# Optimization experiments

Measured on AMD Instinct MI355X. Metric: run time of the kernel, lower is better.

Reference implementation:

```python
import jax, jax.numpy as jnp
import numpy as np

MARGIN = 0.5

def setup_inputs() -> dict:
    key = jax.random.key(0)
    k1, k2 = jax.random.split(key)
    inputs = jax.random.normal(k1, (8192, 256), dtype=jnp.float32)
    target = jax.random.randint(k2, (8192,), 0, 100, dtype=jnp.int64)
    return {"inputs": inputs, "target": target}

def reference(inputs, target):
    N = inputs.shape[0]
    # pairwise squared distances via ||xi||^2 + ||xj||^2 - 2 xi.xj
    sq = jnp.sum(inputs * inputs, axis=1)  # [N]
    gram = inputs @ inputs.T               # [N, N]
    distance = sq[:, None] + sq[None, :] - 2.0 * gram  # [N, N]
    R = (target[None, :] == target[:, None]).astype(inputs.dtype)  # [N, N]
    loss = R * distance + (1.0 - R) * jnp.maximum(MARGIN - distance, 0.0)
    return jnp.sum(loss) / (N * (N - 1.0) * 2.0)
```

## Files before the change

### kernel.cpp

```cpp
#include <hip/hip_runtime.h>
#include <stdint.h>

#define N      8192
#define KDIM   256
#define BM     128
#define TILES  (N / BM)
#define NPAIRS (TILES * (TILES + 1) / 2)
#define MARGIN 0.5f

typedef float f32x4 __attribute__((ext_vector_type(4)));

__device__ __forceinline__ void async_copy16(const void* g, void* l) {
    __builtin_amdgcn_global_load_lds(
        (__attribute__((address_space(1))) void*)(g),
        (__attribute__((address_space(3))) void*)(l),
        16, 0, 0);
}

#if !__has_builtin(__builtin_amdgcn_cvt_pk_fp8_f32)
__device__ __forceinline__ uint32_t f2e4m3(float f) {
    uint32_t u = __float_as_uint(f);
    uint32_t s = (u >> 24) & 0x80u;
    uint32_t au = u & 0x7fffffffu;
    if (au == 0) return s;
    int32_t  exp = (int32_t)(au >> 23) - 127;
    uint32_t man = (au & 0x7fffffu) | 0x800000u;
    uint32_t code;
    if (exp >= -6) {
        code = (uint32_t)((exp + 7) << 3) | ((man >> 20) & 7u);
        uint32_t rem = man & 0xFFFFFu;
        if (rem > 0x80000u || (rem == 0x80000u && (code & 1u))) code++;
    } else {
        int shift = 14 - exp;
        if (shift > 24) return s;
        code = man >> shift;
        uint32_t rem = man & ((1u << shift) - 1u);
        uint32_t h = 1u << (shift - 1);
        if (rem > h || (rem == h && (code & 1u))) code++;
    }
    return s | code;
}
__device__ __forceinline__ uint32_t pack_fp8x4(float4 v) {
    return f2e4m3(v.x) | (f2e4m3(v.y) << 8) | (f2e4m3(v.z) << 16) |
           (f2e4m3(v.w) << 24);
}
#else
__device__ __forceinline__ uint32_t pack_fp8x4(float4 v) {
    int pk = __builtin_amdgcn_cvt_pk_fp8_f32(v.x, v.y, 0, false);
    pk = __builtin_amdgcn_cvt_pk_fp8_f32(v.z, v.w, pk, true);
    return (uint32_t)pk;
}
#endif

__global__ __launch_bounds__(256) void prep_kernel(
        const float* __restrict__ X, uint8_t* __restrict__ Xq,
        float* __restrict__ sq) {
    int row  = blockIdx.x * 4 + (threadIdx.x >> 6);
    int lane = threadIdx.x & 63;

    float4 v = *((const float4*)(X + (size_t)row * KDIM) + lane);
    float ss = v.x * v.x + v.y * v.y + v.z * v.z + v.w * v.w;
    uint32_t pk = pack_fp8x4(v);

    int slot = (lane >> 2) ^ ((row >> 1) & 7);
    *(uint32_t*)(Xq + (size_t)row * KDIM + slot * 16 + (lane & 3) * 4) = pk;

    #pragma unroll
    for (int off = 32; off > 0; off >>= 1) ss += __shfl_down(ss, off, 64);
    if (lane == 0) sq[row] = ss;
}

__global__ __launch_bounds__(256, 2) void loss_kernel(
        const uint8_t* __restrict__ Xq, const float* __restrict__ sq,
        const int* __restrict__ tgt, float* __restrict__ partials) {
    const int p = blockIdx.x;
    float tf = 2.0f * TILES + 1.0f;
    int bi = (int)((tf - sqrtf(tf * tf - 8.0f * (float)p)) * 0.5f);
    if (bi < 0) bi = 0;
    while (bi > 0 && (bi * TILES - bi * (bi - 1) / 2) > p) --bi;
    while (((bi + 1) * TILES - (bi + 1) * bi / 2) <= p) ++bi;
    const int bj = bi + (p - (bi * TILES - bi * (bi - 1) / 2));

    __shared__ __align__(16) uint8_t As[BM * KDIM];
    __shared__ __align__(16) uint8_t Bs[BM * KDIM];
    __shared__ float sqa_s[BM], sqb_s[BM];
    __shared__ int   ta_s[BM],  tb_s[BM];
    __shared__ float wsum[4];

    const int tid  = threadIdx.x;
    const int wave = tid >> 6;
    const int lane = tid & 63;

    if (tid < 128) {
        sqa_s[tid] = sq[bi * BM + tid];
        ta_s[tid]  = tgt[bi * BM + tid];
    } else {
        int r = tid - 128;
        sqb_s[r] = sq[bj * BM + r];
        tb_s[r]  = tgt[bj * BM + r];
    }

    {
        const uint8_t* gA = Xq + ((size_t)bi * BM + wave * 32) * KDIM;
        const uint8_t* gB = Xq + ((size_t)bj * BM + wave * 32) * KDIM;
        uint8_t* lA = As + wave * 32 * KDIM;
        uint8_t* lB = Bs + wave * 32 * KDIM;
        #pragma unroll
        for (int i = 0; i < 8; ++i) {
            async_copy16(gA + i * 1024 + lane * 16, lA + i * 1024);
            async_copy16(gB + i * 1024 + lane * 16, lB + i * 1024);
        }
    }
    __syncthreads();

    const int frow  = lane & 15;
    const int fquad = lane >> 4;
    const int wm = (wave >> 1) * 64;
    const int wn = (wave & 1) * 64;
    const int swz = (frow >> 1) & 7;
    const int fq2 = fquad >> 1;
    const int fqh = (fquad & 1) * 8;

    const uint8_t* abase = As + (wm + frow) * 256 + fqh;
    const uint8_t* bbase = Bs + (wn + frow) * 256 + fqh;

    f32x4 acc[4][4];
    #pragma unroll
    for (int im = 0; im < 4; ++im)
        #pragma unroll
        for (int in = 0; in < 4; ++in)
            acc[im][in] = (f32x4){0.f, 0.f, 0.f, 0.f};

    #pragma unroll
    for (int ks = 0; ks < 8; ++ks) {
        const int t = ((ks * 2 + fq2) ^ swz) * 16;
        long long af[4], bfr[4];
        #pragma unroll
        for (int im = 0; im < 4; ++im)
            af[im] = *(const long long*)(abase + im * 16 * 256 + t);
        #pragma unroll
        for (int in = 0; in < 4; ++in)
            bfr[in] = *(const long long*)(bbase + in * 16 * 256 + t);
        #pragma unroll
        for (int im = 0; im < 4; ++im)
            #pragma unroll
            for (int in = 0; in < 4; ++in)
                acc[im][in] = __builtin_amdgcn_mfma_f32_16x16x32_fp8_fp8(
                    af[im], bfr[in], acc[im][in], 0, 0, 0);
    }

    float lsum = 0.0f;
    if (bi != bj) {
        #pragma unroll
        for (int im = 0; im < 4; ++im) {
            #pragma unroll
            for (int in = 0; in < 4; ++in) {
                #pragma unroll
                for (int r = 0; r < 4; ++r) {
                    int rl = wm + im * 16 + fquad * 4 + r;
                    int cl = wn + in * 16 + frow;
                    float d = fmaf(-2.0f, acc[im][in][r],
                                   sqa_s[rl] + sqb_s[cl]);
                    lsum += (ta_s[rl] == tb_s[cl]) ? d
                                                   : fmaxf(MARGIN - d, 0.0f);
                }
            }
        }
        lsum *= 2.0f;
    } else {
        #pragma unroll
        for (int im = 0; im < 4; ++im) {
            #pragma unroll
            for (int in = 0; in < 4; ++in) {
                #pragma unroll
                for (int r = 0; r < 4; ++r) {
                    int rl = wm + im * 16 + fquad * 4 + r;
                    int cl = wn + in * 16 + frow;
                    float d = fmaf(-2.0f, acc[im][in][r],
                                   sqa_s[rl] + sqb_s[cl]);
                    float c = (ta_s[rl] == tb_s[cl]) ? d
                                                     : fmaxf(MARGIN - d, 0.0f);
                    float w = (rl < cl) ? 2.0f : ((rl == cl) ? 1.0f : 0.0f);
                    lsum += w * c;
                }
            }
        }
    }

    #pragma unroll
    for (int off = 32; off > 0; off >>= 1) lsum += __shfl_down(lsum, off, 64);
    if (lane == 0) wsum[wave] = lsum;
    __syncthreads();
    if (tid == 0) partials[p] = wsum[0] + wsum[1] + wsum[2] + wsum[3];
}

__global__ __launch_bounds__(256) void reduce_kernel(
        const float* __restrict__ partials, float* __restrict__ out,
        int n, float scale) {
    float s = 0.0f;
    for (int i = threadIdx.x; i < n; i += 256) s += partials[i];
    __shared__ float w[4];
    #pragma unroll
    for (int off = 32; off > 0; off >>= 1) s += __shfl_down(s, off, 64);
    int wave = threadIdx.x >> 6, lane = threadIdx.x & 63;
    if (lane == 0) w[wave] = s;
    __syncthreads();
    if (threadIdx.x == 0) out[0] = (w[0] + w[1] + w[2] + w[3]) * scale;
}

extern "C" void kernel_launch(void* const* d_in, const int* in_sizes, int n_in,
                              void* d_out, int out_size, void* d_ws, size_t ws_size,
                              hipStream_t stream) {
    (void)in_sizes; (void)n_in; (void)out_size; (void)ws_size;
    const float* X   = (const float*)d_in[0];
    const int*   tgt = (const int*)d_in[1];

    uint8_t* Xq     = (uint8_t*)d_ws;
    float* sq       = (float*)((char*)d_ws + (size_t)N * KDIM);
    float* partials = sq + N;

    prep_kernel<<<N / 4, 256, 0, stream>>>(X, Xq, sq);
    loss_kernel<<<NPAIRS, 256, 0, stream>>>(Xq, sq, tgt, partials);

    const float scale = (float)(1.0 / ((double)N * ((double)N - 1.0) * 2.0));
    reduce_kernel<<<1, 256, 0, stream>>>(partials, (float*)d_out, NPAIRS, scale);
}
```

Before: 87.46 us.

## Split K into two LDS halves, new fp8 swizzle, raise occupancy to four blocks

```diff
diff --git a/kernel.cpp b/kernel.cpp
--- a/kernel.cpp
+++ b/kernel.cpp
@@ -8,7 +8,8 @@
 #define NPAIRS (TILES * (TILES + 1) / 2)
 #define MARGIN 0.5f
 
-typedef float f32x4 __attribute__((ext_vector_type(4)));
+typedef float     f32x4 __attribute__((ext_vector_type(4)));
+typedef long long i64x2 __attribute__((ext_vector_type(2)));
 
 __device__ __forceinline__ void async_copy16(const void* g, void* l) {
     __builtin_amdgcn_global_load_lds(
@@ -62,15 +63,21 @@
     float ss = v.x * v.x + v.y * v.y + v.z * v.z + v.w * v.w;
     uint32_t pk = pack_fp8x4(v);
 
-    int slot = (lane >> 2) ^ ((row >> 1) & 7);
-    *(uint32_t*)(Xq + (size_t)row * KDIM + slot * 16 + (lane & 3) * 4) = pk;
-
-    #pragma unroll
-    for (int off = 32; off > 0; off >>= 1) ss += __shfl_down(ss, off, 64);
+    int kg = lane * 4;
+    int h  = kg >> 7;
+    int kh = kg & 127;
+    int ks = kh >> 5;
+    int fq = (kh >> 3) & 3;
+    int slot = (fq * 2 + (ks >> 1)) ^ (row & 7);
+    size_t off = (size_t)row * 256 + h * 128 + slot * 16 + (ks & 1) * 8 + (kh & 4);
+    *(uint32_t*)(Xq + off) = pk;
+
+    #pragma unroll
+    for (int o = 32; o > 0; o >>= 1) ss += __shfl_down(ss, o, 64);
     if (lane == 0) sq[row] = ss;
 }
 
-__global__ __launch_bounds__(256, 2) void loss_kernel(
+__global__ __launch_bounds__(256, 4) void loss_kernel(
         const uint8_t* __restrict__ Xq, const float* __restrict__ sq,
         const int* __restrict__ tgt, float* __restrict__ partials) {
     const int p = blockIdx.x;
@@ -81,8 +88,8 @@
     while (((bi + 1) * TILES - (bi + 1) * bi / 2) <= p) ++bi;
     const int bj = bi + (p - (bi * TILES - bi * (bi - 1) / 2));
 
-    __shared__ __align__(16) uint8_t As[BM * KDIM];
-    __shared__ __align__(16) uint8_t Bs[BM * KDIM];
+    __shared__ __align__(16) uint8_t As[BM * 128];
+    __shared__ __align__(16) uint8_t Bs[BM * 128];
     __shared__ float sqa_s[BM], sqb_s[BM];
     __shared__ int   ta_s[BM],  tb_s[BM];
     __shared__ float wsum[4];
@@ -100,29 +107,20 @@
         tb_s[r]  = tgt[bj * BM + r];
     }
 
-    {
-        const uint8_t* gA = Xq + ((size_t)bi * BM + wave * 32) * KDIM;
-        const uint8_t* gB = Xq + ((size_t)bj * BM + wave * 32) * KDIM;
-        uint8_t* lA = As + wave * 32 * KDIM;
-        uint8_t* lB = Bs + wave * 32 * KDIM;
-        #pragma unroll
-        for (int i = 0; i < 8; ++i) {
-            async_copy16(gA + i * 1024 + lane * 16, lA + i * 1024);
-            async_copy16(gB + i * 1024 + lane * 16, lB + i * 1024);
-        }
-    }
-    __syncthreads();
+    const int lrow = lane >> 3;
+    const int lb   = (lane & 7) * 16;
+    const uint8_t* gA0 = Xq + ((size_t)bi * BM + wave * 32 + lrow) * 256 + lb;
+    const uint8_t* gB0 = Xq + ((size_t)bj * BM + wave * 32 + lrow) * 256 + lb;
+    uint8_t* lA = As + wave * 32 * 128;
+    uint8_t* lB = Bs + wave * 32 * 128;
 
     const int frow  = lane & 15;
     const int fquad = lane >> 4;
     const int wm = (wave >> 1) * 64;
     const int wn = (wave & 1) * 64;
-    const int swz = (frow >> 1) & 7;
-    const int fq2 = fquad >> 1;
-    const int fqh = (fquad & 1) * 8;
-
-    const uint8_t* abase = As + (wm + frow) * 256 + fqh;
-    const uint8_t* bbase = Bs + (wn + frow) * 256 + fqh;
+    const int key = frow & 7;
+    const uint8_t* aB = As + (wm + frow) * 128;
+    const uint8_t* bB = Bs + (wn + frow) * 128;
 
     f32x4 acc[4][4];
     #pragma unroll
@@ -132,21 +130,38 @@
             acc[im][in] = (f32x4){0.f, 0.f, 0.f, 0.f};
 
     #pragma unroll
-    for (int ks = 0; ks < 8; ++ks) {
-        const int t = ((ks * 2 + fq2) ^ swz) * 16;
-        long long af[4], bfr[4];
-        #pragma unroll
-        for (int im = 0; im < 4; ++im)
-            af[im] = *(const long long*)(abase + im * 16 * 256 + t);
-        #pragma unroll
-        for (int in = 0; in < 4; ++in)
-            bfr[in] = *(const long long*)(bbase + in * 16 * 256 + t);
-        #pragma unroll
-        for (int im = 0; im < 4; ++im)
+    for (int h = 0; h < 2; ++h) {
+        #pragma unroll
+        for (int q = 0; q < 4; ++q) {
+            async_copy16(gA0 + h * 128 + q * 8 * 256, lA + q * 1024);
+            async_copy16(gB0 + h * 128 + q * 8 * 256, lB + q * 1024);
+        }
+        __syncthreads();
+
+        #pragma unroll
+        for (int ks2 = 0; ks2 < 2; ++ks2) {
+            const int t = ((fquad * 2 + ks2) ^ key) * 16;
+            i64x2 a2[4], b2[4];
+            #pragma unroll
+            for (int im = 0; im < 4; ++im)
+                a2[im] = *(const i64x2*)(aB + im * 16 * 128 + t);
             #pragma unroll
             for (int in = 0; in < 4; ++in)
-                acc[im][in] = __builtin_amdgcn_mfma_f32_16x16x32_fp8_fp8(
-                    af[im], bfr[in], acc[im][in], 0, 0, 0);
+                b2[in] = *(const i64x2*)(bB + in * 16 * 128 + t);
+            #pragma unroll
+            for (int im = 0; im < 4; ++im)
+                #pragma unroll
+                for (int in = 0; in < 4; ++in)
+                    acc[im][in] = __builtin_amdgcn_mfma_f32_16x16x32_fp8_fp8(
+                        a2[im].x, b2[in].x, acc[im][in], 0, 0, 0);
+            #pragma unroll
+            for (int im = 0; im < 4; ++im)
+                #pragma unroll
+                for (int in = 0; in < 4; ++in)
+                    acc[im][in] = __builtin_amdgcn_mfma_f32_16x16x32_fp8_fp8(
+                        a2[im].y, b2[in].y, acc[im][in], 0, 0, 0);
+        }
+        if (h == 0) __syncthreads();
     }
 
     float lsum = 0.0f;
@@ -188,7 +203,7 @@
     }
 
     #pragma unroll
-    for (int off = 32; off > 0; off >>= 1) lsum += __shfl_down(lsum, off, 64);
+    for (int o = 32; o > 0; o >>= 1) lsum += __shfl_down(lsum, o, 64);
     if (lane == 0) wsum[wave] = lsum;
     __syncthreads();
     if (tid == 0) partials[p] = wsum[0] + wsum[1] + wsum[2] + wsum[3];
@@ -201,7 +216,7 @@
     for (int i = threadIdx.x; i < n; i += 256) s += partials[i];
     __shared__ float w[4];
     #pragma unroll
-    for (int off = 32; off > 0; off >>= 1) s += __shfl_down(s, off, 64);
+    for (int o = 32; o > 0; o >>= 1) s += __shfl_down(s, o, 64);
     int wave = threadIdx.x >> 6, lane = threadIdx.x & 63;
     if (lane == 0) w[wave] = s;
     __syncthreads();
```

After: 80.74 us. 1.08x faster.

## Pipeline K-chunks with double-buffered LDS and fuse final reduction via atomics

Applied to the files above, without the earlier changes.

```diff
diff --git a/kernel.cpp b/kernel.cpp
--- a/kernel.cpp
+++ b/kernel.cpp
@@ -7,8 +7,10 @@
 #define TILES  (N / BM)
 #define NPAIRS (TILES * (TILES + 1) / 2)
 #define MARGIN 0.5f
-
-typedef float f32x4 __attribute__((ext_vector_type(4)));
+#define PS     ((size_t)N * 64)
+
+typedef float     f32x4 __attribute__((ext_vector_type(4)));
+typedef long long i64x2 __attribute__((ext_vector_type(2)));
 
 __device__ __forceinline__ void async_copy16(const void* g, void* l) {
     __builtin_amdgcn_global_load_lds(
@@ -54,7 +56,7 @@
 
 __global__ __launch_bounds__(256) void prep_kernel(
         const float* __restrict__ X, uint8_t* __restrict__ Xq,
-        float* __restrict__ sq) {
+        float* __restrict__ sq, float* __restrict__ out) {
     int row  = blockIdx.x * 4 + (threadIdx.x >> 6);
     int lane = threadIdx.x & 63;
 
@@ -62,17 +64,19 @@
     float ss = v.x * v.x + v.y * v.y + v.z * v.z + v.w * v.w;
     uint32_t pk = pack_fp8x4(v);
 
-    int slot = (lane >> 2) ^ ((row >> 1) & 7);
-    *(uint32_t*)(Xq + (size_t)row * KDIM + slot * 16 + (lane & 3) * 4) = pk;
+    int c = lane >> 4;
+    int p = (lane * 4) & 63;
+    *(uint32_t*)(Xq + (size_t)c * PS + (size_t)row * 64 + p) = pk;
 
     #pragma unroll
-    for (int off = 32; off > 0; off >>= 1) ss += __shfl_down(ss, off, 64);
+    for (int o = 32; o > 0; o >>= 1) ss += __shfl_down(ss, o, 64);
     if (lane == 0) sq[row] = ss;
-}
-
-__global__ __launch_bounds__(256, 2) void loss_kernel(
+    if (blockIdx.x == 0 && threadIdx.x == 0) out[0] = 0.0f;
+}
+
+__global__ __launch_bounds__(256, 4) void loss_kernel(
         const uint8_t* __restrict__ Xq, const float* __restrict__ sq,
-        const int* __restrict__ tgt, float* __restrict__ partials) {
+        const int* __restrict__ tgt, float* __restrict__ out) {
     const int p = blockIdx.x;
     float tf = 2.0f * TILES + 1.0f;
     int bi = (int)((tf - sqrtf(tf * tf - 8.0f * (float)p)) * 0.5f);
@@ -81,8 +85,8 @@
     while (((bi + 1) * TILES - (bi + 1) * bi / 2) <= p) ++bi;
     const int bj = bi + (p - (bi * TILES - bi * (bi - 1) / 2));
 
-    __shared__ __align__(16) uint8_t As[BM * KDIM];
-    __shared__ __align__(16) uint8_t Bs[BM * KDIM];
+    __shared__ __align__(16) uint8_t As[2][BM * 64];
+    __shared__ __align__(16) uint8_t Bs[2][BM * 64];
     __shared__ float sqa_s[BM], sqb_s[BM];
     __shared__ int   ta_s[BM],  tb_s[BM];
     __shared__ float wsum[4];
@@ -100,29 +104,22 @@
         tb_s[r]  = tgt[bj * BM + r];
     }
 
-    {
-        const uint8_t* gA = Xq + ((size_t)bi * BM + wave * 32) * KDIM;
-        const uint8_t* gB = Xq + ((size_t)bj * BM + wave * 32) * KDIM;
-        uint8_t* lA = As + wave * 32 * KDIM;
-        uint8_t* lB = Bs + wave * 32 * KDIM;
-        #pragma unroll
-        for (int i = 0; i < 8; ++i) {
-            async_copy16(gA + i * 1024 + lane * 16, lA + i * 1024);
-            async_copy16(gB + i * 1024 + lane * 16, lB + i * 1024);
-        }
-    }
-    __syncthreads();
+    const uint8_t* gA = Xq + ((size_t)bi * BM + wave * 32) * 64 + lane * 16;
+    const uint8_t* gB = Xq + ((size_t)bj * BM + wave * 32) * 64 + lane * 16;
+    uint8_t* lA0 = &As[0][wave * 2048];
+    uint8_t* lA1 = &As[1][wave * 2048];
+    uint8_t* lB0 = &Bs[0][wave * 2048];
+    uint8_t* lB1 = &Bs[1][wave * 2048];
 
     const int frow  = lane & 15;
     const int fquad = lane >> 4;
     const int wm = (wave >> 1) * 64;
     const int wn = (wave & 1) * 64;
-    const int swz = (frow >> 1) & 7;
-    const int fq2 = fquad >> 1;
-    const int fqh = (fquad & 1) * 8;
-
-    const uint8_t* abase = As + (wm + frow) * 256 + fqh;
-    const uint8_t* bbase = Bs + (wn + frow) * 256 + fqh;
+
+    const uint8_t* aB0 = &As[0][(wm + frow) * 64 + fquad * 16];
+    const uint8_t* bB0 = &Bs[0][(wn + frow) * 64 + fquad * 16];
+    const uint8_t* aB1 = &As[1][(wm + frow) * 64 + fquad * 16];
+    const uint8_t* bB1 = &Bs[1][(wn + frow) * 64 + fquad * 16];
 
     f32x4 acc[4][4];
     #pragma unroll
@@ -131,23 +128,52 @@
         for (int in = 0; in < 4; ++in)
             acc[im][in] = (f32x4){0.f, 0.f, 0.f, 0.f};
 
-    #pragma unroll
-    for (int ks = 0; ks < 8; ++ks) {
-        const int t = ((ks * 2 + fq2) ^ swz) * 16;
-        long long af[4], bfr[4];
-        #pragma unroll
-        for (int im = 0; im < 4; ++im)
-            af[im] = *(const long long*)(abase + im * 16 * 256 + t);
-        #pragma unroll
-        for (int in = 0; in < 4; ++in)
-            bfr[in] = *(const long long*)(bbase + in * 16 * 256 + t);
-        #pragma unroll
-        for (int im = 0; im < 4; ++im)
-            #pragma unroll
-            for (int in = 0; in < 4; ++in)
-                acc[im][in] = __builtin_amdgcn_mfma_f32_16x16x32_fp8_fp8(
-                    af[im], bfr[in], acc[im][in], 0, 0, 0);
-    }
+    #define STAGE(c, la, lb)                                                 \
+        do {                                                                 \
+            async_copy16(gA + (size_t)(c) * PS,        (la));                \
+            async_copy16(gA + (size_t)(c) * PS + 1024, (la) + 1024);         \
+            async_copy16(gB + (size_t)(c) * PS,        (lb));                \
+            async_copy16(gB + (size_t)(c) * PS + 1024, (lb) + 1024);         \
+        } while (0)
+
+    #define COMPUTE(ab, bb)                                                  \
+        do {                                                                 \
+            i64x2 a2[4], b2[4];                                              \
+            _Pragma("unroll")                                                \
+            for (int im = 0; im < 4; ++im)                                   \
+                a2[im] = *(const i64x2*)((ab) + im * 16 * 64);               \
+            _Pragma("unroll")                                                \
+            for (int in = 0; in < 4; ++in)                                   \
+                b2[in] = *(const i64x2*)((bb) + in * 16 * 64);               \
+            _Pragma("unroll")                                                \
+            for (int im = 0; im < 4; ++im)                                   \
+                _Pragma("unroll")                                            \
+                for (int in = 0; in < 4; ++in)                               \
+                    acc[im][in] = __builtin_amdgcn_mfma_f32_16x16x32_fp8_fp8(\
+                        a2[im].x, b2[in].x, acc[im][in], 0, 0, 0);           \
+            _Pragma("unroll")                                                \
+            for (int im = 0; im < 4; ++im)                                   \
+                _Pragma("unroll")                                            \
+                for (int in = 0; in < 4; ++in)                               \
+                    acc[im][in] = __builtin_amdgcn_mfma_f32_16x16x32_fp8_fp8(\
+                        a2[im].y, b2[in].y, acc[im][in], 0, 0, 0);           \
+        } while (0)
+
+    STAGE(0, lA0, lB0);
+    __syncthreads();
+    STAGE(1, lA1, lB1);
+    COMPUTE(aB0, bB0);
+    __syncthreads();
+    STAGE(2, lA0, lB0);
+    COMPUTE(aB1, bB1);
+    __syncthreads();
+    STAGE(3, lA1, lB1);
+    COMPUTE(aB0, bB0);
+    __syncthreads();
+    COMPUTE(aB1, bB1);
+
+    #undef STAGE
+    #undef COMPUTE
 
     float lsum = 0.0f;
     if (bi != bj) {
@@ -188,24 +214,14 @@
     }
 
     #pragma unroll
-    for (int off = 32; off > 0; off >>= 1) lsum += __shfl_down(lsum, off, 64);
+    for (int o = 32; o > 0; o >>= 1) lsum += __shfl_down(lsum, o, 64);
     if (lane == 0) wsum[wave] = lsum;
     __syncthreads();
-    if (tid == 0) partials[p] = wsum[0] + wsum[1] + wsum[2] + wsum[3];
-}
-
-__global__ __launch_bounds__(256) void reduce_kernel(
-        const float* __restrict__ partials, float* __restrict__ out,
-        int n, float scale) {
-    float s = 0.0f;
-    for (int i = threadIdx.x; i < n; i += 256) s += partials[i];
-    __shared__ float w[4];
-    #pragma unroll
-    for (int off = 32; off > 0; off >>= 1) s += __shfl_down(s, off, 64);
-    int wave = threadIdx.x >> 6, lane = threadIdx.x & 63;
-    if (lane == 0) w[wave] = s;
-    __syncthreads();
-    if (threadIdx.x == 0) out[0] = (w[0] + w[1] + w[2] + w[3]) * scale;
+    if (tid == 0) {
+        const float scale =
+            (float)(1.0 / ((double)N * ((double)N - 1.0) * 2.0));
+        atomicAdd(out, (wsum[0] + wsum[1] + wsum[2] + wsum[3]) * scale);
+    }
 }
 
 extern "C" void kernel_launch(void* const* d_in, const int* in_sizes, int n_in,
@@ -215,13 +231,9 @@
     const float* X   = (const float*)d_in[0];
     const int*   tgt = (const int*)d_in[1];
 
-    uint8_t* Xq     = (uint8_t*)d_ws;
-    float* sq       = (float*)((char*)d_ws + (size_t)N * KDIM);
-    float* partials = sq + N;
-
-    prep_kernel<<<N / 4, 256, 0, stream>>>(X, Xq, sq);
-    loss_kernel<<<NPAIRS, 256, 0, stream>>>(Xq, sq, tgt, partials);
-
-    const float scale = (float)(1.0 / ((double)N * ((double)N - 1.0) * 2.0));
-    reduce_kernel<<<1, 256, 0, stream>>>(partials, (float*)d_out, NPAIRS, scale);
-}
+    uint8_t* Xq = (uint8_t*)d_ws;
+    float*   sq = (float*)((char*)d_ws + (size_t)N * KDIM);
+
+    prep_kernel<<<N / 4, 256, 0, stream>>>(X, Xq, sq, (float*)d_out);
+    loss_kernel<<<NPAIRS, 256, 0, stream>>>(Xq, sq, tgt, (float*)d_out);
+}
```

Result: slower. 94.66 us (+8.2%).
